# Kernel tuning notes

Hardware: AMD Instinct MI355X
Metric: run time of the kernel (lower is better)

## Reference

```python
import jax, jax.numpy as jnp
import numpy as np

BS = 2048   # batch, iterated sequentially (memory carried step to step)
M = 256     # memory_size
E = 128     # expanded_memory_emb_size
HS = 512    # summarizer_hidden_size
HA = 512    # shared_AC_hidden_size
HP = 256    # processor_hidden_size


def make_pe(max_len, d):
    # standard sinusoidal positional encoding [max_len, d]
    pos = np.arange(max_len, dtype=np.float32)[:, None]
    div = np.exp(np.arange(0, d, 2, dtype=np.float32) * (-np.log(10000.0) / d))
    pe = np.zeros((max_len, d), dtype=np.float32)
    pe[:, 0::2] = np.sin(pos * div)
    pe[:, 1::2] = np.cos(pos * div)
    return jnp.asarray(pe)


def setup_inputs() -> dict:
    key = jax.random.key(0)
    ks = jax.random.split(key, 32)

    def n(k, sh, s=0.05):
        return jax.random.normal(k, sh, dtype=jnp.float32) * s

    return {
        "state": jax.random.normal(ks[0], (BS, 4), dtype=jnp.float32),
        "memory0": jax.random.uniform(ks[1], (M, E), dtype=jnp.float32),  # buffer init U(0,1)
        # embedder: Linear(4, E)
        "W_emb": n(ks[2], (4, E)), "b_emb": n(ks[3], (E,)),
        # reader Summarizer MLP: E -> HS -> 1
        "Wr1": n(ks[4], (E, HS)), "br1": n(ks[5], (HS,)),
        "Wr2": n(ks[6], (HS, 1)), "br2": n(ks[7], (1,)),
        # writer Summarizer MLP: E -> HS -> M
        "Ww1": n(ks[8], (E, HS)), "bw1": n(ks[9], (HS,)),
        "Ww2": n(ks[10], (HS, M)), "bw2": n(ks[11], (M,)),
        # shared AC trunk: 2E -> HA
        "Ws": n(ks[12], (2 * E, HA)), "bs_": n(ks[13], (HA,)),
        # actor: HA -> 5, critic: HA -> 1
        "Wa": n(ks[14], (HA, 5)), "ba": n(ks[15], (5,)),
        "Wc": n(ks[16], (HA, 1)), "bc": n(ks[17], (1,)),
        # processor: (5 + 1 + 2E) -> HP -> E
        "Wp1": n(ks[18], (5 + 1 + 2 * E, HP)), "bp1": n(ks[19], (HP,)),
        "Wp2": n(ks[20], (HP, E)), "bp2": n(ks[21], (E,)),
    }


def reference(state, memory0, W_emb, b_emb, Wr1, br1, Wr2, br2,
              Ww1, bw1, Ww2, bw2, Ws, bs_, Wa, ba, Wc, bc,
              Wp1, bp1, Wp2, bp2):
    pe_mem = make_pe(M, E)  # PE added to the M memory slots
    sg = jax.lax.stop_gradient

    def summarize(x, W1, b1, W2, b2):
        # Summarizer (MLP method): weight = softmax over token axis, z = weight^T x
        w = jax.nn.softmax(jax.nn.relu(x @ W1 + b1) @ W2 + b2, axis=0)  # [T, K]
        return w.T @ x  # [K, E]

    se = state @ W_emb + b_emb  # embed once: [BS, E]

    def step(mem, s):
        # reader over [current state ; PE(memory)] -> single summary token
        xr = jnp.concatenate([s[None, :], mem + pe_mem], axis=0)        # [M+1, E]
        mem_state = summarize(xr, Wr1, br1, Wr2, br2)[0]                # [E]
        cstate = jnp.concatenate([s, mem_state])                        # concat=True -> [2E]
        h = jax.nn.relu(cstate @ Ws + bs_)                              # [HA]
        probs = jax.nn.softmax(h @ Wa + ba)                             # [5]
        val = h @ Wc + bc                                               # [1]
        pin = jnp.concatenate([s, mem_state, probs, val])               # [2E+6]
        ms2 = jax.nn.relu(pin @ Wp1 + bp1) @ Wp2 + bp2                  # processed mem_state [E]
        # writer sees detached state / mem_state / memory (torch .detach())
        xw = jnp.concatenate([sg(s)[None, :], sg(ms2)[None, :], sg(mem) + pe_mem], axis=0)  # [M+2, E]
        nm = summarize(xw, Ww1, bw1, Ww2, bw2)                          # [M, E]
        nm = nm - nm.min(axis=-1, keepdims=True)
        nm = nm / nm.max(axis=-1, keepdims=True)
        return nm, (probs, val)

    _, (action_probs, state_values) = jax.lax.scan(step, memory0, se)
    return action_probs, state_values  # [BS, 5], [BS, 1]
```

## Files before the change

### kernel.cpp

```cpp
#include <hip/hip_runtime.h>
#include <math.h>

#define BSZ 2048
#define MM  256
#define EE  128
#define HSS 512
#define HPP 256
#define NOWN 64
#define NBLK 129
#define LEADER 128
#define TPB 512
#define ROWS 4

typedef float f4 __attribute__((ext_vector_type(4)));

#define OFF_PE   512
#define OFF_R0   (OFF_PE + MM*EE)
#define OFF_W0   (OFF_R0 + BSZ)
#define OFF_MP   (OFF_W0 + BSZ*MM)
#define OFF_SW   (OFF_MP + 2*MM*EE)
#define OFF_EV   (OFF_SW + 2*MM*MM)
#define OFF_ES   (OFF_EV + NOWN*EE)
#define OFF_MS2  (OFF_ES + NOWN)
#define OFF_CS   (OFF_MS2 + EE)
#define OFF_CBS  (OFF_CS + 4*HSS)
#define OFF_CP   (OFF_CBS + HSS)
#define OFF_CBP  (OFF_CP + 4*HPP)
#define OFF_BD   (OFF_CBP + HPP)
#define OFF_BP   (OFF_BD + NOWN*ROWS)
#define OFF_PWR  (OFF_BP + NOWN*ROWS*EE)
#define OFF_PWW  (OFF_PWR + MM*HSS)
#define OFF_CSR  (OFF_PWW + MM*HSS)
#define OFF_CSW  (OFF_CSR + HSS)
#define OFF_CR   (OFF_CSW + HSS)
#define OFF_CBR  (OFF_CR + 4*HSS)
#define OFF_CW2  (OFF_CBR + HSS)
#define OFF_CBW  (OFF_CW2 + 4*HSS)
#define OFF_MSR  (OFF_CBW + HSS)
#define OFF_MSW  (OFF_MSR + 2*HSS)
#define OFF_SCAL (OFF_MSW + 2*HSS)

struct KParams {
  const float *state, *mem0, *Wemb, *bemb, *Wr1, *br1, *Wr2, *br2;
  const float *Ww1, *bw1, *Ww2, *bw2, *Ws, *bs, *Wa, *ba, *Wc, *bc;
  const float *Wp1, *bp1, *Wp2, *bp2;
  float *out;
  float *ws;
};

__device__ __forceinline__ float ldA(const float* p) {
  return __hip_atomic_load(p, __ATOMIC_RELAXED, __HIP_MEMORY_SCOPE_AGENT);
}
__device__ __forceinline__ void stA(float* p, float v) {
  __hip_atomic_store(p, v, __ATOMIC_RELAXED, __HIP_MEMORY_SCOPE_AGENT);
}
__device__ __forceinline__ unsigned ldAu(const unsigned* p) {
  return __hip_atomic_load(p, __ATOMIC_RELAXED, __HIP_MEMORY_SCOPE_AGENT);
}
__device__ __forceinline__ void stAu(unsigned* p, unsigned v) {
  __hip_atomic_store(p, v, __ATOMIC_RELAXED, __HIP_MEMORY_SCOPE_AGENT);
}

__device__ __forceinline__ void ldA4x8(const float* p, int strideF, f4* v) {
  const float *p1=p+strideF, *p2=p+2*strideF, *p3=p+3*strideF,
              *p4=p+4*strideF, *p5=p+5*strideF, *p6=p+6*strideF, *p7=p+7*strideF;
  asm volatile(
    "global_load_dwordx4 %0, %8, off sc0 sc1\n\t"
    "global_load_dwordx4 %1, %9, off sc0 sc1\n\t"
    "global_load_dwordx4 %2, %10, off sc0 sc1\n\t"
    "global_load_dwordx4 %3, %11, off sc0 sc1\n\t"
    "global_load_dwordx4 %4, %12, off sc0 sc1\n\t"
    "global_load_dwordx4 %5, %13, off sc0 sc1\n\t"
    "global_load_dwordx4 %6, %14, off sc0 sc1\n\t"
    "global_load_dwordx4 %7, %15, off sc0 sc1\n\t"
    "s_waitcnt vmcnt(0)"
    : "=&v"(v[0]), "=&v"(v[1]), "=&v"(v[2]), "=&v"(v[3]),
      "=&v"(v[4]), "=&v"(v[5]), "=&v"(v[6]), "=&v"(v[7])
    : "v"(p), "v"(p1), "v"(p2), "v"(p3), "v"(p4), "v"(p5), "v"(p6), "v"(p7)
    : "memory");
}
__device__ __forceinline__ void ldA4x4(const float* p, int strideF, f4* v) {
  const float *p1=p+strideF, *p2=p+2*strideF, *p3=p+3*strideF;
  asm volatile(
    "global_load_dwordx4 %0, %4, off sc0 sc1\n\t"
    "global_load_dwordx4 %1, %5, off sc0 sc1\n\t"
    "global_load_dwordx4 %2, %6, off sc0 sc1\n\t"
    "global_load_dwordx4 %3, %7, off sc0 sc1\n\t"
    "s_waitcnt vmcnt(0)"
    : "=&v"(v[0]), "=&v"(v[1]), "=&v"(v[2]), "=&v"(v[3])
    : "v"(p), "v"(p1), "v"(p2), "v"(p3)
    : "memory");
}
__device__ __forceinline__ f4 ldA4(const float* p) {
  f4 r;
  asm volatile("global_load_dwordx4 %0, %1, off sc0 sc1\n\ts_waitcnt vmcnt(0)"
    : "=&v"(r) : "v"(p) : "memory");
  return r;
}

__device__ __forceinline__ void drainSync() {
  asm volatile("s_waitcnt vmcnt(0)" ::: "memory");
  __syncthreads();
}

__device__ __forceinline__ float brs(float v, float* s8, int tid) {
  for (int o = 32; o > 0; o >>= 1) v += __shfl_down(v, o, 64);
  __syncthreads();
  if ((tid & 63) == 0) s8[tid >> 6] = v;
  __syncthreads();
  float r = s8[0]+s8[1]+s8[2]+s8[3]+s8[4]+s8[5]+s8[6]+s8[7];
  __syncthreads();
  return r;
}

template<int N>
__device__ __forceinline__ void brsN(float* v, float* sred, int tid) {
  #pragma unroll
  for (int k = 0; k < N; ++k)
    for (int o = 32; o > 0; o >>= 1) v[k] += __shfl_down(v[k], o, 64);
  __syncthreads();
  if ((tid & 63) == 0) {
    const int w = tid >> 6;
    #pragma unroll
    for (int k = 0; k < N; ++k) sred[k*8 + w] = v[k];
  }
  __syncthreads();
  #pragma unroll
  for (int k = 0; k < N; ++k) {
    float s = sred[k*8 + 0];
    #pragma unroll
    for (int w = 1; w < 8; ++w) s += sred[k*8 + w];
    v[k] = s;
  }
  __syncthreads();
}

__global__ __launch_bounds__(TPB)
void toyac_kernel(KParams p) {
  const int g = blockIdx.x;
  const int tid = threadIdx.x;
  float* ws = p.ws;
  unsigned* bar = (unsigned*)p.ws;
  const int og = (g >= NOWN && g < LEADER) ? (g - NOWN) : g;
  const int c0 = ROWS * ((g < NOWN) ? g : og);

  __shared__ float sBuf[8192];
  __shared__ float sX[ROWS][EE];
  __shared__ float sP[ROWS][EE];
  __shared__ float sPE[ROWS][EE];
  __shared__ float sPW[ROWS][HSS];
  __shared__ float sH4[ROWS][HSS];
  __shared__ float sMSR[HSS];
  __shared__ float sMSWv[HSS];
  __shared__ float sRed[16];
  __shared__ float s8[8];
  __shared__ float sR48[48];
  __shared__ float sMS[EE];
  __shared__ float sMS2[EE];
  __shared__ float sSE[EE];
  __shared__ float sP1[HPP];
  __shared__ float sD[ROWS];
  __shared__ float sSm[40];

  float (*sEv)[MM] = (float(*)[MM])sH4;
  float* sHv = &sH4[2][0];

  const int hq = (tid & 127) * 4;
  const int eg4 = tid >> 7;

  auto streamPW = [&](const float* W, float (*src)[EE]) {
    {
      f4 a0={0.f,0.f,0.f,0.f},a1=a0,a2=a0,a3=a0;
      const float* base = W + (size_t)(eg4*32)*HSS + hq;
      for (int i = 0; i < 32; ++i) {
        f4 w = *(const f4*)(base + (size_t)i*HSS);
        int e = eg4*32 + i;
        a0 += src[0][e]*w; a1 += src[1][e]*w; a2 += src[2][e]*w; a3 += src[3][e]*w;
      }
      *(f4*)(sBuf + ((size_t)eg4*ROWS + 0)*HSS + hq) = a0;
      *(f4*)(sBuf + ((size_t)eg4*ROWS + 1)*HSS + hq) = a1;
      *(f4*)(sBuf + ((size_t)eg4*ROWS + 2)*HSS + hq) = a2;
      *(f4*)(sBuf + ((size_t)eg4*ROWS + 3)*HSS + hq) = a3;
    }
    __syncthreads();
    #pragma unroll
    for (int r = 0; r < ROWS; ++r)
      sPW[r][tid] = sBuf[(0*ROWS+r)*HSS+tid] + sBuf[(1*ROWS+r)*HSS+tid]
                  + sBuf[(2*ROWS+r)*HSS+tid] + sBuf[(3*ROWS+r)*HSS+tid];
    __syncthreads();
  };

  if (g < NOWN) {
    const int e = tid & 127, r = tid >> 7, c = c0 + r;
    double dv = exp(-(double)(2*(e>>1)) * log(10000.0) / 128.0);
    double arg = (double)c * dv;
    float pev = ((e & 1) == 0) ? (float)sin(arg) : (float)cos(arg);
    stA(ws + OFF_PE + (size_t)c*EE + e, pev);
    sPE[r][e] = pev;
    float m0v = p.mem0[(size_t)c*EE + e] + pev;
    stA(ws + OFF_MP + (size_t)c*EE + e, m0v);
    sX[r][e] = m0v;
  } else if (g == LEADER) {
    for (int jj = tid; jj < HSS; jj += TPB) {
      float a0=0.f,a1=0.f,a2=0.f,a3=0.f,cb=0.f;
      for (int e = 0; e < EE; ++e) {
        float wv = p.Ws[(size_t)e*HSS + jj];
        a0 += p.Wemb[e]*wv; a1 += p.Wemb[EE+e]*wv;
        a2 += p.Wemb[2*EE+e]*wv; a3 += p.Wemb[3*EE+e]*wv;
        cb += p.bemb[e]*wv;
      }
      ws[OFF_CS + jj] = a0; ws[OFF_CS + HSS + jj] = a1;
      ws[OFF_CS + 2*HSS + jj] = a2; ws[OFF_CS + 3*HSS + jj] = a3;
      ws[OFF_CBS + jj] = cb;
    }
    if (tid < HPP) {
      int k = tid;
      float a0=0.f,a1=0.f,a2=0.f,a3=0.f,cb=0.f;
      for (int e = 0; e < EE; ++e) {
        float wv = p.Wp1[(size_t)e*HPP + k];
        a0 += p.Wemb[e]*wv; a1 += p.Wemb[EE+e]*wv;
        a2 += p.Wemb[2*EE+e]*wv; a3 += p.Wemb[3*EE+e]*wv;
        cb += p.bemb[e]*wv;
      }
      ws[OFF_CP + k] = a0; ws[OFF_CP + HPP + k] = a1;
      ws[OFF_CP + 2*HPP + k] = a2; ws[OFF_CP + 3*HPP + k] = a3;
      ws[OFF_CBP + k] = cb;
    }
    {
      int j = tid;
      float r0=0.f,r1=0.f,r2=0.f,r3=0.f,rb=0.f,rc=0.f;
      float w0=0.f,w1=0.f,w2=0.f,w3=0.f,wb=0.f,wc=0.f;
      for (int e = 0; e < EE; ++e) {
        float wr = p.Wr1[(size_t)e*HSS + j];
        float ww = p.Ww1[(size_t)e*HSS + j];
        float we0=p.Wemb[e], we1=p.Wemb[EE+e], we2=p.Wemb[2*EE+e], we3=p.Wemb[3*EE+e], wbe=p.bemb[e];
        r0+=we0*wr; r1+=we1*wr; r2+=we2*wr; r3+=we3*wr; rb+=wbe*wr; rc+=wr;
        w0+=we0*ww; w1+=we1*ww; w2+=we2*ww; w3+=we3*ww; wb+=wbe*ww; wc+=ww;
      }
      stA(ws+OFF_CR+j, r0); stA(ws+OFF_CR+HSS+j, r1);
      stA(ws+OFF_CR+2*HSS+j, r2); stA(ws+OFF_CR+3*HSS+j, r3);
      stA(ws+OFF_CBR+j, rb); stA(ws+OFF_CSR+j, rc);
      stA(ws+OFF_CW2+j, w0); stA(ws+OFF_CW2+HSS+j, w1);
      stA(ws+OFF_CW2+2*HSS+j, w2); stA(ws+OFF_CW2+3*HSS+j, w3);
      stA(ws+OFF_CBW+j, wb); stA(ws+OFF_CSW+j, wc);
    }
  }

  for (int t = g; t < BSZ; t += NBLK) {
    __syncthreads();
    if (tid < EE) {
      const float* st = p.state + (size_t)t*4;
      sSE[tid] = st[0]*p.Wemb[tid] + st[1]*p.Wemb[EE+tid]
               + st[2]*p.Wemb[2*EE+tid] + st[3]*p.Wemb[3*EE+tid] + p.bemb[tid];
    }
    __syncthreads();
    {
      f4 a = {0.f,0.f,0.f,0.f};
      const float* base = p.Wr1 + (size_t)(eg4*32)*HSS + hq;
      for (int i = 0; i < 32; ++i)
        a += sSE[eg4*32 + i] * (*(const f4*)(base + (size_t)i*HSS));
      *(f4*)(sBuf + (size_t)eg4*HSS + hq) = a;
      __syncthreads();
      int h = tid;
      float hid = sBuf[h] + sBuf[HSS+h] + sBuf[2*HSS+h] + sBuf[3*HSS+h] + p.br1[h];
      float v = fmaxf(hid, 0.f) * p.Wr2[h];
      float sc = brs(v, s8, tid);
      if (tid == 0) stA(ws + OFF_R0 + t, sc + p.br2[0]);
      __syncthreads();
    }
    {
      f4 a = {0.f,0.f,0.f,0.f};
      const float* base = p.Ww1 + (size_t)(eg4*32)*HSS + hq;
      for (int i = 0; i < 32; ++i)
        a += sSE[eg4*32 + i] * (*(const f4*)(base + (size_t)i*HSS));
      *(f4*)(sBuf + (size_t)eg4*HSS + hq) = a;
      __syncthreads();
      int h = tid;
      sHv[h] = fmaxf(sBuf[h] + sBuf[HSS+h] + sBuf[2*HSS+h] + sBuf[3*HSS+h] + p.bw1[h], 0.f);
      __syncthreads();
      const int cq = (tid & 63) * 4, hg = tid >> 6;
      f4 q = {0.f,0.f,0.f,0.f};
      const float* b2 = p.Ww2 + (size_t)(hg*64)*MM + cq;
      for (int i = 0; i < 64; ++i)
        q += sHv[hg*64 + i] * (*(const f4*)(b2 + (size_t)i*MM));
      *(f4*)(sBuf + (size_t)hg*MM + cq) = q;
      __syncthreads();
      if (tid < MM) {
        float s = 0.f;
        #pragma unroll
        for (int k = 0; k < 8; ++k) s += sBuf[(size_t)k*MM + tid];
        stA(ws + OFF_W0 + (size_t)t*MM + tid, s + p.bw2[tid]);
      }
      __syncthreads();
    }
  }

  auto stageA_full = [&]() {
    {
      f4 a0={0.f,0.f,0.f,0.f},a1=a0,a2=a0,a3=a0;
      const float* base = p.Wr1 + (size_t)(eg4*32)*HSS + hq;
      for (int i = 0; i < 32; ++i) {
        f4 w = *(const f4*)(base + (size_t)i*HSS);
        int e = eg4*32 + i;
        a0 += sX[0][e]*w; a1 += sX[1][e]*w; a2 += sX[2][e]*w; a3 += sX[3][e]*w;
      }
      *(f4*)(sBuf + ((size_t)eg4*ROWS + 0)*HSS + hq) = a0;
      *(f4*)(sBuf + ((size_t)eg4*ROWS + 1)*HSS + hq) = a1;
      *(f4*)(sBuf + ((size_t)eg4*ROWS + 2)*HSS + hq) = a2;
      *(f4*)(sBuf + ((size_t)eg4*ROWS + 3)*HSS + hq) = a3;
    }
    __syncthreads();
    float es[ROWS];
    {
      int h = tid;
      float b = p.br1[h], wr = p.Wr2[h];
      float sc[ROWS];
      #pragma unroll
      for (int r = 0; r < ROWS; ++r) {
        float hid = sBuf[(0*ROWS+r)*HSS+h] + sBuf[(1*ROWS+r)*HSS+h]
                  + sBuf[(2*ROWS+r)*HSS+h] + sBuf[(3*ROWS+r)*HSS+h] + b;
        sc[r] = fmaxf(hid, 0.f) * wr;
      }
      brsN<ROWS>(sc, sR48, tid);
      #pragma unroll
      for (int r = 0; r < ROWS; ++r) es[r] = expf(sc[r] + p.br2[0]);
    }
    if (tid < EE) {
      float v = es[0]*sX[0][tid] + es[1]*sX[1][tid] + es[2]*sX[2][tid] + es[3]*sX[3][tid];
      stA(ws + OFF_EV + (size_t)g*EE + tid, v);
    }
    if (tid == 0) stA(ws + OFF_ES + g, es[0]+es[1]+es[2]+es[3]);
  };

  auto ww2pass = [&](float* swdst) {
    const int cq = (tid & 63) * 4, hg = tid >> 6;
    f4 q0={0.f,0.f,0.f,0.f},q1=q0,q2=q0,q3=q0;
    const float* b2 = p.Ww2 + (size_t)(hg*64)*MM + cq;
    for (int i = 0; i < 64; ++i) {
      f4 w = *(const f4*)(b2 + (size_t)i*MM);
      int h = hg*64 + i;
      q0 += sH4[0][h]*w; q1 += sH4[1][h]*w; q2 += sH4[2][h]*w; q3 += sH4[3][h]*w;
    }
    *(f4*)(sBuf + ((size_t)hg*ROWS + 0)*MM + cq) = q0;
    *(f4*)(sBuf + ((size_t)hg*ROWS + 1)*MM + cq) = q1;
    *(f4*)(sBuf + ((size_t)hg*ROWS + 2)*MM + cq) = q2;
    *(f4*)(sBuf + ((size_t)hg*ROWS + 3)*MM + cq) = q3;
    __syncthreads();
    {
      const int col = tid & 255, rp = tid >> 8;
      #pragma unroll
      for (int rr = 0; rr < 2; ++rr) {
        int r = rp*2 + rr;
        float s = 0.f;
        #pragma unroll
        for (int k = 0; k < 8; ++k) s += sBuf[((size_t)k*ROWS + r)*MM + col];
        stA(swdst + (size_t)(c0 + r)*MM + col, s + p.bw2[col]);
      }
    }
  };

  auto stageC_full = [&](float* swdst) {
    {
      f4 a0={0.f,0.f,0.f,0.f},a1=a0,a2=a0,a3=a0;
      const float* base = p.Ww1 + (size_t)(eg4*32)*HSS + hq;
      for (int i = 0; i < 32; ++i) {
        f4 w = *(const f4*)(base + (size_t)i*HSS);
        int e = eg4*32 + i;
        a0 += sX[0][e]*w; a1 += sX[1][e]*w; a2 += sX[2][e]*w; a3 += sX[3][e]*w;
      }
      *(f4*)(sBuf + ((size_t)eg4*ROWS + 0)*HSS + hq) = a0;
      *(f4*)(sBuf + ((size_t)eg4*ROWS + 1)*HSS + hq) = a1;
      *(f4*)(sBuf + ((size_t)eg4*ROWS + 2)*HSS + hq) = a2;
      *(f4*)(sBuf + ((size_t)eg4*ROWS + 3)*HSS + hq) = a3;
    }
    __syncthreads();
    {
      int h = tid;
      float b = p.bw1[h];
      #pragma unroll
      for (int r = 0; r < ROWS; ++r)
        sH4[r][h] = fmaxf(sBuf[(0*ROWS+r)*HSS+h] + sBuf[(1*ROWS+r)*HSS+h]
                        + sBuf[(2*ROWS+r)*HSS+h] + sBuf[(3*ROWS+r)*HSS+h] + b, 0.f);
    }
    __syncthreads();
    ww2pass(swdst);
  };

  auto dBulkH = [&](int tt) {
    float* swc = ws + OFF_SW + (size_t)(tt&1)*MM*MM;
    float* mpc = ws + OFF_MP + (size_t)(tt&1)*MM*EE;
    float ex[ROWS] = {0.f,0.f,0.f,0.f};
    if (tid < MM) {
      f4 s = ldA4(swc + (size_t)tid*MM + c0);
      #pragma unroll
      for (int r = 0; r < ROWS; ++r) { ex[r] = expf(s[r]); sEv[r][tid] = ex[r]; }
    }
    brsN<ROWS>(ex, sR48, tid);
    if (tid == 0) {
      stA(ws + OFF_BD + og*ROWS + 0, ex[0]);
      stA(ws + OFF_BD + og*ROWS + 1, ex[1]);
      stA(ws + OFF_BD + og*ROWS + 2, ex[2]);
      stA(ws + OFF_BD + og*ROWS + 3, ex[3]);
    }
    {
      const int e4 = (tid & 31) * 4, rg = tid >> 5;
      f4 a0={0.f,0.f,0.f,0.f},a1=a0,a2=a0,a3=a0;
      const float* base = mpc + (size_t)(rg*16)*EE + e4;
      f4 vv[8];
      ldA4x8(base, EE, vv);
      #pragma unroll
      for (int i = 0; i < 8; ++i) {
        int r0 = rg*16 + i;
        a0 += sEv[0][r0]*vv[i]; a1 += sEv[1][r0]*vv[i];
        a2 += sEv[2][r0]*vv[i]; a3 += sEv[3][r0]*vv[i];
      }
      ldA4x8(base + 8*EE, EE, vv);
      #pragma unroll
      for (int i = 0; i < 8; ++i) {
        int r0 = rg*16 + 8 + i;
        a0 += sEv[0][r0]*vv[i]; a1 += sEv[1][r0]*vv[i];
        a2 += sEv[2][r0]*vv[i]; a3 += sEv[3][r0]*vv[i];
      }
      *(f4*)(sBuf + ((size_t)0*16 + rg)*EE + e4) = a0;
      *(f4*)(sBuf + ((size_t)1*16 + rg)*EE + e4) = a1;
      *(f4*)(sBuf + ((size_t)2*16 + rg)*EE + e4) = a2;
      *(f4*)(sBuf + ((size_t)3*16 + rg)*EE + e4) = a3;
    }
    __syncthreads();
    {
      const int e = tid & 127, r = tid >> 7;
      float s = 0.f;
      #pragma unroll
      for (int q = 0; q < 16; ++q) s += sBuf[((size_t)r*16 + q)*EE + e];
      sP[r][e] = s;
      stA(ws + OFF_BP + ((size_t)og*ROWS + r)*EE + e, s);
    }
    __syncthreads();
  };

  if (g == LEADER) {
    for (int t = 0; t < BSZ; ++t) {
      if (tid < NOWN) {
        while (ldAu(&bar[64+tid]) < (unsigned)(t+1)) __builtin_amdgcn_s_sleep(1);
      }
      __syncthreads();
      const float* st = p.state + (size_t)t*4;
      const float s0 = st[0], s1 = st[1], s2 = st[2], s3 = st[3];
      if (tid < EE)
        sSE[tid] = s0*p.Wemb[tid] + s1*p.Wemb[EE+tid]
                 + s2*p.Wemb[2*EE+tid] + s3*p.Wemb[3*EE+tid] + p.bemb[tid];
      float er0 = expf(ldA(ws + OFF_R0 + t));
      float v = (tid < NOWN) ? ldA(ws + OFF_ES + tid) : 0.f;
      float invd = 1.f / (er0 + brs(v, s8, tid));
      {
        const int e4 = (tid & 31) * 4, qg = tid >> 5;
        f4 vv[4];
        ldA4x4(ws + OFF_EV + (size_t)(qg*4)*EE + e4, EE, vv);
        f4 acc = vv[0]+vv[1]+vv[2]+vv[3];
        *(f4*)(sBuf + (size_t)qg*EE + e4) = acc;
      }
      __syncthreads();
      if (tid < EE) {
        float s = 0.f;
        #pragma unroll
        for (int q = 0; q < 16; ++q) s += sBuf[(size_t)q*EE + tid];
        sMS[tid] = (er0*sSE[tid] + s) * invd;
      }
      __syncthreads();
      {
        f4 a = {0.f,0.f,0.f,0.f};
        const float* base = p.Ws + (size_t)(EE + eg4*32)*HSS + hq;
        for (int i = 0; i < 32; ++i)
          a += sMS[eg4*32 + i] * (*(const f4*)(base + (size_t)i*HSS));
        *(f4*)(sBuf + (size_t)eg4*HSS + hq) = a;
      }
      __syncthreads();
      float hv;
      {
        int j = tid;
        const float* cs = ws + OFF_CS;
        float sh0 = s0*cs[j] + s1*cs[HSS+j] + s2*cs[2*HSS+j] + s3*cs[3*HSS+j] + ws[OFF_CBS + j];
        hv = fmaxf(sBuf[j] + sBuf[HSS+j] + sBuf[2*HSS+j] + sBuf[3*HSS+j] + sh0 + p.bs[j], 0.f);
      }
      __syncthreads();
      {
        int j = tid;
        float pa[6];
        #pragma unroll
        for (int aa = 0; aa < 5; ++aa) pa[aa] = hv * p.Wa[(size_t)j*5 + aa];
        pa[5] = hv * p.Wc[j];
        brsN<6>(pa, sR48, tid);
        if (tid == 0) {
          float l0=pa[0]+p.ba[0], l1=pa[1]+p.ba[1], l2=pa[2]+p.ba[2];
          float l3=pa[3]+p.ba[3], l4=pa[4]+p.ba[4];
          float mx = fmaxf(fmaxf(fmaxf(l0,l1),fmaxf(l2,l3)), l4);
          float e0=expf(l0-mx),e1=expf(l1-mx),e2=expf(l2-mx),e3=expf(l3-mx),e4v=expf(l4-mx);
          float is = 1.f/(e0+e1+e2+e3+e4v);
          float p0=e0*is,p1=e1*is,p2=e2*is,p3=e3*is,p4=e4v*is;
          p.out[(size_t)t*5+0]=p0; p.out[(size_t)t*5+1]=p1; p.out[(size_t)t*5+2]=p2;
          p.out[(size_t)t*5+3]=p3; p.out[(size_t)t*5+4]=p4;
          float val = pa[5] + p.bc[0];
          p.out[(size_t)BSZ*5 + t] = val;
          sSm[1]=p0; sSm[2]=p1; sSm[3]=p2; sSm[4]=p3; sSm[5]=p4; sSm[6]=val;
        }
        __syncthreads();
      }
      {
        const int cq = (tid & 63) * 4, eg8 = tid >> 6;
        f4 a = {0.f,0.f,0.f,0.f};
        const float* base = p.Wp1 + (size_t)(EE + eg8*16)*HPP + cq;
        for (int i = 0; i < 16; ++i)
          a += sMS[eg8*16 + i] * (*(const f4*)(base + (size_t)i*HPP));
        *(f4*)(sBuf + (size_t)eg8*HPP + cq) = a;
      }
      __syncthreads();
      if (tid < HPP) {
        int k = tid;
        const float* cp = ws + OFF_CP;
        float acc = s0*cp[k] + s1*cp[HPP+k] + s2*cp[2*HPP+k] + s3*cp[3*HPP+k]
                  + ws[OFF_CBP + k] + p.bp1[k];
        #pragma unroll
        for (int q = 0; q < 8; ++q) acc += sBuf[(size_t)q*HPP + k];
        #pragma unroll
        for (int aa = 0; aa < 5; ++aa) acc += sSm[1+aa] * p.Wp1[(size_t)(2*EE+aa)*HPP + k];
        acc += sSm[6] * p.Wp1[(size_t)(2*EE+5)*HPP + k];
        sP1[k] = fmaxf(acc, 0.f);
      }
      __syncthreads();
      {
        const int cq = (tid & 31) * 4, kg = tid >> 5;
        f4 a = {0.f,0.f,0.f,0.f};
        const float* base = p.Wp2 + (size_t)(kg*16)*EE + cq;
        for (int i = 0; i < 16; ++i)
          a += sP1[kg*16 + i] * (*(const f4*)(base + (size_t)i*EE));
        *(f4*)(sBuf + (size_t)kg*EE + cq) = a;
      }
      __syncthreads();
      if (tid < EE) {
        float s = 0.f;
        #pragma unroll
        for (int q = 0; q < 16; ++q) s += sBuf[(size_t)q*EE + tid];
        stA(ws + OFF_MS2 + tid, s + p.bp2[tid]);
      }
      drainSync();
      if (tid == 0) stAu(&bar[320], (unsigned)(t+1));
    }
  } else if (g < NOWN) {
    const f4 wcol = *(const f4*)(p.Ww2 + (size_t)tid*MM + c0);
    drainSync();
    if (tid == 0) stAu(&bar[g], 1u);
    streamPW(p.Wr1, sPE);
    #pragma unroll
    for (int r = 0; r < ROWS; ++r)
      ws[OFF_PWR + (size_t)(c0+r)*HSS + tid] = sPW[r][tid];
    __syncthreads();
    stageA_full();
    drainSync();
    if (tid == 0) stAu(&bar[64+g], 1u);

    for (int t = 0; t < BSZ-1; ++t) {
      if (tid == 0) {
        while (ldAu(&bar[320]) < (unsigned)(t+1)) __builtin_amdgcn_s_sleep(1);
      }
      __syncthreads();
      if (tid < EE) sMS2[tid] = ldA(ws + OFF_MS2 + tid);
      __syncthreads();
      {
        const int h8 = tid >> 6, ee = tid & 63;
        const int h = 8*g + h8;
        float m1 = sMS2[ee], m2 = sMS2[ee+64];
        float pr = m1*p.Wr1[(size_t)ee*HSS+h] + m2*p.Wr1[(size_t)(ee+64)*HSS+h];
        float pw = m1*p.Ww1[(size_t)ee*HSS+h] + m2*p.Ww1[(size_t)(ee+64)*HSS+h];
        for (int o = 32; o > 0; o >>= 1) {
          pr += __shfl_down(pr, o, 64);
          pw += __shfl_down(pw, o, 64);
        }
        if (ee == 0) {
          stA(ws + OFF_MSR + (size_t)(t&1)*HSS + h, pr);
          stA(ws + OFF_MSW + (size_t)(t&1)*HSS + h, pw);
        }
      }
      drainSync();
      if (tid == 0) stAu(&bar[256+g], (unsigned)(t+1));
      if (tid == 0) {
        while (ldAu(&bar[192+g]) < (unsigned)(t+1)) __builtin_amdgcn_s_sleep(1);
      }
      __syncthreads();
      if (tid == 0) {
        f4 d = ldA4(ws + OFF_BD + g*ROWS);
        sD[0]=d.x; sD[1]=d.y; sD[2]=d.z; sD[3]=d.w;
        f4 w0 = ldA4(ws + OFF_W0 + (size_t)t*MM + c0);
        sSm[8+0]=expf(w0.x); sSm[8+1]=expf(w0.y); sSm[8+2]=expf(w0.z); sSm[8+3]=expf(w0.w);
      }
      {
        const int e = tid & 127, r = tid >> 7;
        sP[r][e] = ldA(ws + OFF_BP + ((size_t)g*ROWS + r)*EE + e);
      }
      __syncthreads();
      streamPW(p.Wr1, sP);
      if (tid < NOWN) {
        while (ldAu(&bar[256+tid]) < (unsigned)(t+1)) __builtin_amdgcn_s_sleep(1);
      }
      __syncthreads();
      sMSR[tid]  = ldA(ws + OFF_MSR + (size_t)(t&1)*HSS + tid);
      sMSWv[tid] = ldA(ws + OFF_MSW + (size_t)(t&1)*HSS + tid);
      __syncthreads();
      float swv[ROWS];
      {
        float hm = fmaxf(sMSWv[tid] + p.bw1[tid], 0.f);
        swv[0]=hm*wcol.x; swv[1]=hm*wcol.y; swv[2]=hm*wcol.z; swv[3]=hm*wcol.w;
        brsN<ROWS>(swv, sR48, tid);
      }
      const float* st = p.state + (size_t)t*4;
      {
        const int e = tid & 127, r = tid >> 7;
        float ew1 = expf(swv[r] + p.bw2[c0+r]);
        float ew0 = sSm[8+r];
        float inv = 1.f / (sD[r] + ew0 + ew1);
        float se = st[0]*p.Wemb[e] + st[1]*p.Wemb[EE+e]
                 + st[2]*p.Wemb[2*EE+e] + st[3]*p.Wemb[3*EE+e] + p.bemb[e];
        float x = (sP[r][e] + ew0*se + ew1*sMS2[e]) * inv;
        float mn = x, mx = x;
        #pragma unroll
        for (int o = 1; o < 64; o <<= 1) {
          mn = fminf(mn, __shfl_xor(mn, o, 64));
          mx = fmaxf(mx, __shfl_xor(mx, o, 64));
        }
        if ((tid & 63) == 0) { sRed[(tid>>6)*2] = mn; sRed[(tid>>6)*2+1] = mx; }
        __syncthreads();
        mn = fminf(sRed[4*r], sRed[4*r+2]);
        mx = fmaxf(sRed[4*r+1], sRed[4*r+3]);
        float k = 1.f / (mx - mn);
        float xr = (x - mn) * k + sPE[r][e];
        float* mpn = ws + OFF_MP + (size_t)((t+1)&1)*MM*EE;
        stA(mpn + (size_t)(c0+r)*EE + e, xr);
        sX[r][e] = xr;
        if (tid < 4) {
          int rr = tid;
          float ew1b = expf(swv[rr] + p.bw2[c0+rr]);
          float invb = 1.f / (sD[rr] + sSm[8+rr] + ew1b);
          float mnb = fminf(sRed[4*rr], sRed[4*rr+2]);
          float mxb = fmaxf(sRed[4*rr+1], sRed[4*rr+3]);
          float kb = 1.f / (mxb - mnb);
          float a = kb * invb;
          float b = a * sSm[8+rr];
          float c = a * ew1b;
          float d = -mnb * kb;
          stA(ws + OFF_SCAL + (size_t)(c0+rr)*4 + 0, a);
          stA(ws + OFF_SCAL + (size_t)(c0+rr)*4 + 1, b);
          stA(ws + OFF_SCAL + (size_t)(c0+rr)*4 + 2, c);
          stA(ws + OFF_SCAL + (size_t)(c0+rr)*4 + 3, d);
          sSm[16+rr*4+0]=a; sSm[16+rr*4+1]=b; sSm[16+rr*4+2]=c; sSm[16+rr*4+3]=d;
        }
      }
      drainSync();
      if (tid == 0) stAu(&bar[g], (unsigned)(t+2));
      {
        const int j = tid;
        float seW = st[0]*ldA(ws+OFF_CR+j) + st[1]*ldA(ws+OFF_CR+HSS+j)
                  + st[2]*ldA(ws+OFF_CR+2*HSS+j) + st[3]*ldA(ws+OFF_CR+3*HSS+j)
                  + ldA(ws+OFF_CBR+j);
        float csv = ldA(ws+OFF_CSR+j);
        float br = p.br1[j], wr = p.Wr2[j];
        float sc[ROWS];
        #pragma unroll
        for (int r = 0; r < ROWS; ++r) {
          float pre = sSm[16+r*4+0]*sPW[r][j] + sSm[16+r*4+1]*seW
                    + sSm[16+r*4+2]*sMSR[j] + sSm[16+r*4+3]*csv
                    + ws[OFF_PWR + (size_t)(c0+r)*HSS + j] + br;
          sc[r] = fmaxf(pre, 0.f) * wr;
        }
        brsN<ROWS>(sc, sR48, tid);
        float es[ROWS];
        #pragma unroll
        for (int r = 0; r < ROWS; ++r) es[r] = expf(sc[r] + p.br2[0]);
        if (tid < EE) {
          float v = es[0]*sX[0][tid] + es[1]*sX[1][tid] + es[2]*sX[2][tid] + es[3]*sX[3][tid];
          stA(ws + OFF_EV + (size_t)g*EE + tid, v);
        }
        if (tid == 0) stA(ws + OFF_ES + g, es[0]+es[1]+es[2]+es[3]);
      }
      drainSync();
      if (tid == 0) stAu(&bar[64+g], (unsigned)(t+2));
    }
  } else {
    if (tid == 0) {
      while (ldAu(&bar[og]) < 1u) __builtin_amdgcn_s_sleep(1);
    }
    __syncthreads();
    {
      const int e = tid & 127, r = tid >> 7;
      sPE[r][e] = ldA(ws + OFF_PE + (size_t)(c0+r)*EE + e);
      sX[r][e]  = ldA(ws + OFF_MP + (size_t)(c0+r)*EE + e);
    }
    __syncthreads();
    streamPW(p.Ww1, sPE);
    #pragma unroll
    for (int r = 0; r < ROWS; ++r)
      ws[OFF_PWW + (size_t)(c0+r)*HSS + tid] = sPW[r][tid];
    __syncthreads();
    stageC_full(ws + OFF_SW);
    drainSync();
    if (tid == 0) stAu(&bar[128+og], 1u);
    if (tid < 64) {
      while (ldAu(&bar[128+tid]) < 1u) __builtin_amdgcn_s_sleep(1);
    } else if (tid < 128) {
      while (ldAu(&bar[tid-64]) < 1u) __builtin_amdgcn_s_sleep(1);
    }
    __syncthreads();
    dBulkH(0);
    drainSync();
    if (tid == 0) stAu(&bar[192+og], 1u);
    streamPW(p.Ww1, sP);

    for (int t = 0; t < BSZ-2; ++t) {
      if (tid < NOWN) {
        while (ldAu(&bar[256+tid]) < (unsigned)(t+1)) __builtin_amdgcn_s_sleep(1);
      }
      __syncthreads();
      sMSWv[tid] = ldA(ws + OFF_MSW + (size_t)(t&1)*HSS + tid);
      if (tid == 0) {
        while (ldAu(&bar[og]) < (unsigned)(t+2)) __builtin_amdgcn_s_sleep(1);
      }
      __syncthreads();
      if (tid < 16) sSm[16+tid] = ldA(ws + OFF_SCAL + (size_t)c0*4 + tid);
      __syncthreads();
      {
        const int j = tid;
        const float* st = p.state + (size_t)t*4;
        float seW = st[0]*ldA(ws+OFF_CW2+j) + st[1]*ldA(ws+OFF_CW2+HSS+j)
                  + st[2]*ldA(ws+OFF_CW2+2*HSS+j) + st[3]*ldA(ws+OFF_CW2+3*HSS+j)
                  + ldA(ws+OFF_CBW+j);
        float csv = ldA(ws+OFF_CSW+j);
        float bw = p.bw1[j];
        #pragma unroll
        for (int r = 0; r < ROWS; ++r) {
          float pre = sSm[16+r*4+0]*sPW[r][j] + sSm[16+r*4+1]*seW
                    + sSm[16+r*4+2]*sMSWv[j] + sSm[16+r*4+3]*csv
                    + ws[OFF_PWW + (size_t)(c0+r)*HSS + j] + bw;
          sH4[r][j] = fmaxf(pre, 0.f);
        }
      }
      __syncthreads();
      ww2pass(ws + OFF_SW + (size_t)((t+1)&1)*MM*MM);
      drainSync();
      if (tid == 0) stAu(&bar[128+og], (unsigned)(t+2));
      if (tid < 64) {
        while (ldAu(&bar[128+tid]) < (unsigned)(t+2)) __builtin_amdgcn_s_sleep(1);
      } else if (tid < 128) {
        while (ldAu(&bar[tid-64]) < (unsigned)(t+2)) __builtin_amdgcn_s_sleep(1);
      }
      __syncthreads();
      dBulkH(t+1);
      drainSync();
      if (tid == 0) stAu(&bar[192+og], (unsigned)(t+2));
      streamPW(p.Ww1, sP);
    }
  }
}

extern "C" void kernel_launch(void* const* d_in, const int* in_sizes, int n_in,
                              void* d_out, int out_size, void* d_ws, size_t ws_size,
                              hipStream_t stream) {
  hipMemsetAsync(d_ws, 0, 2048, stream);
  KParams kp;
  kp.state = (const float*)d_in[0];
  kp.mem0  = (const float*)d_in[1];
  kp.Wemb  = (const float*)d_in[2];
  kp.bemb  = (const float*)d_in[3];
  kp.Wr1   = (const float*)d_in[4];
  kp.br1   = (const float*)d_in[5];
  kp.Wr2   = (const float*)d_in[6];
  kp.br2   = (const float*)d_in[7];
  kp.Ww1   = (const float*)d_in[8];
  kp.bw1   = (const float*)d_in[9];
  kp.Ww2   = (const float*)d_in[10];
  kp.bw2   = (const float*)d_in[11];
  kp.Ws    = (const float*)d_in[12];
  kp.bs    = (const float*)d_in[13];
  kp.Wa    = (const float*)d_in[14];
  kp.ba    = (const float*)d_in[15];
  kp.Wc    = (const float*)d_in[16];
  kp.bc    = (const float*)d_in[17];
  kp.Wp1   = (const float*)d_in[18];
  kp.bp1   = (const float*)d_in[19];
  kp.Wp2   = (const float*)d_in[20];
  kp.bp2   = (const float*)d_in[21];
  kp.out   = (float*)d_out;
  kp.ws    = (float*)d_ws;
  toyac_kernel<<<dim3(NBLK), dim3(TPB), 0, stream>>>(kp);
}
```

Measured before the change: 57.19 ms.

## Remove leader block, replicate controller in owners, offload reader projection to helpers

Drops the dedicated leader block so every owner block recomputes the per-step actor-critic/processor path redundantly, with block 0 writing outputs. The reader's projection of P through Wr1 moves to the helper blocks, which publish it in a new workspace buffer. EV/ES become double-buffered and the per-step constants are hoisted into registers. The intent is to remove the leader-to-owner barrier hop from each sequential step's critical path. In exchange, every owner does redundant work and the barrier protocol is reorganised, which risks new ordering bugs.

```diff
diff --git a/kernel.cpp b/kernel.cpp
--- a/kernel.cpp
+++ b/kernel.cpp
@@ -7,38 +7,37 @@
 #define HSS 512
 #define HPP 256
 #define NOWN 64
-#define NBLK 129
-#define LEADER 128
+#define NBLK 128
 #define TPB 512
 #define ROWS 4
 
 typedef float f4 __attribute__((ext_vector_type(4)));
 
-#define OFF_PE   512
-#define OFF_R0   (OFF_PE + MM*EE)
-#define OFF_W0   (OFF_R0 + BSZ)
-#define OFF_MP   (OFF_W0 + BSZ*MM)
-#define OFF_SW   (OFF_MP + 2*MM*EE)
-#define OFF_EV   (OFF_SW + 2*MM*MM)
-#define OFF_ES   (OFF_EV + NOWN*EE)
-#define OFF_MS2  (OFF_ES + NOWN)
-#define OFF_CS   (OFF_MS2 + EE)
-#define OFF_CBS  (OFF_CS + 4*HSS)
-#define OFF_CP   (OFF_CBS + HSS)
-#define OFF_CBP  (OFF_CP + 4*HPP)
-#define OFF_BD   (OFF_CBP + HPP)
-#define OFF_BP   (OFF_BD + NOWN*ROWS)
-#define OFF_PWR  (OFF_BP + NOWN*ROWS*EE)
-#define OFF_PWW  (OFF_PWR + MM*HSS)
-#define OFF_CSR  (OFF_PWW + MM*HSS)
-#define OFF_CSW  (OFF_CSR + HSS)
-#define OFF_CR   (OFF_CSW + HSS)
-#define OFF_CBR  (OFF_CR + 4*HSS)
-#define OFF_CW2  (OFF_CBR + HSS)
-#define OFF_CBW  (OFF_CW2 + 4*HSS)
-#define OFF_MSR  (OFF_CBW + HSS)
-#define OFF_MSW  (OFF_MSR + 2*HSS)
-#define OFF_SCAL (OFF_MSW + 2*HSS)
+#define OFF_PE    512
+#define OFF_R0    (OFF_PE + MM*EE)
+#define OFF_W0    (OFF_R0 + BSZ)
+#define OFF_MP    (OFF_W0 + BSZ*MM)
+#define OFF_SW    (OFF_MP + 2*MM*EE)
+#define OFF_EV    (OFF_SW + 2*MM*MM)
+#define OFF_ES    (OFF_EV + 2*NOWN*EE)
+#define OFF_CS    (OFF_ES + 2*NOWN)
+#define OFF_CBS   (OFF_CS + 4*HSS)
+#define OFF_CP    (OFF_CBS + HSS)
+#define OFF_CBP   (OFF_CP + 4*HPP)
+#define OFF_CR    (OFF_CBP + HPP)
+#define OFF_CBR   (OFF_CR + 4*HSS)
+#define OFF_CSR   (OFF_CBR + HSS)
+#define OFF_CW2   (OFF_CSR + HSS)
+#define OFF_CBW   (OFF_CW2 + 4*HSS)
+#define OFF_CSW   (OFF_CBW + HSS)
+#define OFF_BD    (OFF_CSW + HSS)
+#define OFF_BP    (OFF_BD + NOWN*ROWS)
+#define OFF_PWRD  (OFF_BP + NOWN*ROWS*EE)
+#define OFF_PWRpe (OFF_PWRD + NOWN*ROWS*HSS)
+#define OFF_PWWpe (OFF_PWRpe + MM*HSS)
+#define OFF_MSR   (OFF_PWWpe + MM*HSS)
+#define OFF_MSW   (OFF_MSR + 2*HSS)
+#define OFF_SCAL  (OFF_MSW + 2*HSS)
 
 struct KParams {
   const float *state, *mem0, *Wemb, *bemb, *Wr1, *br1, *Wr2, *br2;
@@ -141,29 +140,30 @@
   const int tid = threadIdx.x;
   float* ws = p.ws;
   unsigned* bar = (unsigned*)p.ws;
-  const int og = (g >= NOWN && g < LEADER) ? (g - NOWN) : g;
-  const int c0 = ROWS * ((g < NOWN) ? g : og);
+  const int isOwner = (g < NOWN);
+  const int og = isOwner ? g : (g - NOWN);
+  const int c0 = ROWS * og;
 
   __shared__ float sBuf[8192];
+  __shared__ float sPW[ROWS][HSS];
+  __shared__ float sH4[ROWS][HSS];
   __shared__ float sX[ROWS][EE];
   __shared__ float sP[ROWS][EE];
   __shared__ float sPE[ROWS][EE];
-  __shared__ float sPW[ROWS][HSS];
-  __shared__ float sH4[ROWS][HSS];
   __shared__ float sMSR[HSS];
   __shared__ float sMSWv[HSS];
-  __shared__ float sRed[16];
-  __shared__ float s8[8];
-  __shared__ float sR48[48];
   __shared__ float sMS[EE];
   __shared__ float sMS2[EE];
   __shared__ float sSE[EE];
   __shared__ float sP1[HPP];
   __shared__ float sD[ROWS];
+  __shared__ float sR48[48];
+  __shared__ float s8[8];
+  __shared__ float sRed[16];
   __shared__ float sSm[40];
 
   float (*sEv)[MM] = (float(*)[MM])sH4;
-  float* sHv = &sH4[2][0];
+  float* sHv = sMSR;
 
   const int hq = (tid & 127) * 4;
   const int eg4 = tid >> 7;
@@ -190,7 +190,7 @@
     __syncthreads();
   };
 
-  if (g < NOWN) {
+  if (isOwner) {
     const int e = tid & 127, r = tid >> 7, c = c0 + r;
     double dv = exp(-(double)(2*(e>>1)) * log(10000.0) / 128.0);
     double arg = (double)c * dv;
@@ -200,49 +200,50 @@
     float m0v = p.mem0[(size_t)c*EE + e] + pev;
     stA(ws + OFF_MP + (size_t)c*EE + e, m0v);
     sX[r][e] = m0v;
-  } else if (g == LEADER) {
-    for (int jj = tid; jj < HSS; jj += TPB) {
-      float a0=0.f,a1=0.f,a2=0.f,a3=0.f,cb=0.f;
-      for (int e = 0; e < EE; ++e) {
-        float wv = p.Ws[(size_t)e*HSS + jj];
-        a0 += p.Wemb[e]*wv; a1 += p.Wemb[EE+e]*wv;
-        a2 += p.Wemb[2*EE+e]*wv; a3 += p.Wemb[3*EE+e]*wv;
-        cb += p.bemb[e]*wv;
-      }
-      ws[OFF_CS + jj] = a0; ws[OFF_CS + HSS + jj] = a1;
-      ws[OFF_CS + 2*HSS + jj] = a2; ws[OFF_CS + 3*HSS + jj] = a3;
-      ws[OFF_CBS + jj] = cb;
-    }
-    if (tid < HPP) {
-      int k = tid;
-      float a0=0.f,a1=0.f,a2=0.f,a3=0.f,cb=0.f;
-      for (int e = 0; e < EE; ++e) {
-        float wv = p.Wp1[(size_t)e*HPP + k];
-        a0 += p.Wemb[e]*wv; a1 += p.Wemb[EE+e]*wv;
-        a2 += p.Wemb[2*EE+e]*wv; a3 += p.Wemb[3*EE+e]*wv;
-        cb += p.bemb[e]*wv;
-      }
-      ws[OFF_CP + k] = a0; ws[OFF_CP + HPP + k] = a1;
-      ws[OFF_CP + 2*HPP + k] = a2; ws[OFF_CP + 3*HPP + k] = a3;
-      ws[OFF_CBP + k] = cb;
-    }
-    {
+    if (g == 0) {
       int j = tid;
-      float r0=0.f,r1=0.f,r2=0.f,r3=0.f,rb=0.f,rc=0.f;
-      float w0=0.f,w1=0.f,w2=0.f,w3=0.f,wb=0.f,wc=0.f;
-      for (int e = 0; e < EE; ++e) {
-        float wr = p.Wr1[(size_t)e*HSS + j];
-        float ww = p.Ww1[(size_t)e*HSS + j];
-        float we0=p.Wemb[e], we1=p.Wemb[EE+e], we2=p.Wemb[2*EE+e], we3=p.Wemb[3*EE+e], wbe=p.bemb[e];
-        r0+=we0*wr; r1+=we1*wr; r2+=we2*wr; r3+=we3*wr; rb+=wbe*wr; rc+=wr;
-        w0+=we0*ww; w1+=we1*ww; w2+=we2*ww; w3+=we3*ww; wb+=wbe*ww; wc+=ww;
-      }
-      stA(ws+OFF_CR+j, r0); stA(ws+OFF_CR+HSS+j, r1);
-      stA(ws+OFF_CR+2*HSS+j, r2); stA(ws+OFF_CR+3*HSS+j, r3);
-      stA(ws+OFF_CBR+j, rb); stA(ws+OFF_CSR+j, rc);
-      stA(ws+OFF_CW2+j, w0); stA(ws+OFF_CW2+HSS+j, w1);
-      stA(ws+OFF_CW2+2*HSS+j, w2); stA(ws+OFF_CW2+3*HSS+j, w3);
-      stA(ws+OFF_CBW+j, wb); stA(ws+OFF_CSW+j, wc);
+      {
+        float a0=0.f,a1=0.f,a2=0.f,a3=0.f,cb=0.f;
+        for (int ee = 0; ee < EE; ++ee) {
+          float wv = p.Ws[(size_t)ee*HSS + j];
+          a0 += p.Wemb[ee]*wv; a1 += p.Wemb[EE+ee]*wv;
+          a2 += p.Wemb[2*EE+ee]*wv; a3 += p.Wemb[3*EE+ee]*wv;
+          cb += p.bemb[ee]*wv;
+        }
+        stA(ws+OFF_CS+j, a0); stA(ws+OFF_CS+HSS+j, a1);
+        stA(ws+OFF_CS+2*HSS+j, a2); stA(ws+OFF_CS+3*HSS+j, a3);
+        stA(ws+OFF_CBS+j, cb);
+      }
+      {
+        float r0=0.f,r1=0.f,r2=0.f,r3=0.f,rb=0.f,rc=0.f;
+        float w0=0.f,w1=0.f,w2=0.f,w3=0.f,wb=0.f,wc=0.f;
+        for (int ee = 0; ee < EE; ++ee) {
+          float wr = p.Wr1[(size_t)ee*HSS + j];
+          float wwv = p.Ww1[(size_t)ee*HSS + j];
+          float we0=p.Wemb[ee], we1=p.Wemb[EE+ee], we2=p.Wemb[2*EE+ee], we3=p.Wemb[3*EE+ee], wbe=p.bemb[ee];
+          r0+=we0*wr; r1+=we1*wr; r2+=we2*wr; r3+=we3*wr; rb+=wbe*wr; rc+=wr;
+          w0+=we0*wwv; w1+=we1*wwv; w2+=we2*wwv; w3+=we3*wwv; wb+=wbe*wwv; wc+=wwv;
+        }
+        stA(ws+OFF_CR+j, r0); stA(ws+OFF_CR+HSS+j, r1);
+        stA(ws+OFF_CR+2*HSS+j, r2); stA(ws+OFF_CR+3*HSS+j, r3);
+        stA(ws+OFF_CBR+j, rb); stA(ws+OFF_CSR+j, rc);
+        stA(ws+OFF_CW2+j, w0); stA(ws+OFF_CW2+HSS+j, w1);
+        stA(ws+OFF_CW2+2*HSS+j, w2); stA(ws+OFF_CW2+3*HSS+j, w3);
+        stA(ws+OFF_CBW+j, wb); stA(ws+OFF_CSW+j, wc);
+      }
+      if (tid < HPP) {
+        int k = tid;
+        float a0=0.f,a1=0.f,a2=0.f,a3=0.f,cb=0.f;
+        for (int ee = 0; ee < EE; ++ee) {
+          float wv = p.Wp1[(size_t)ee*HPP + k];
+          a0 += p.Wemb[ee]*wv; a1 += p.Wemb[EE+ee]*wv;
+          a2 += p.Wemb[2*EE+ee]*wv; a3 += p.Wemb[3*EE+ee]*wv;
+          cb += p.bemb[ee]*wv;
+        }
+        stA(ws+OFF_CP+k, a0); stA(ws+OFF_CP+HPP+k, a1);
+        stA(ws+OFF_CP+2*HPP+k, a2); stA(ws+OFF_CP+3*HPP+k, a3);
+        stA(ws+OFF_CBP+k, cb);
+      }
     }
   }
 
@@ -294,43 +295,6 @@
       __syncthreads();
     }
   }
-
-  auto stageA_full = [&]() {
-    {
-      f4 a0={0.f,0.f,0.f,0.f},a1=a0,a2=a0,a3=a0;
-      const float* base = p.Wr1 + (size_t)(eg4*32)*HSS + hq;
-      for (int i = 0; i < 32; ++i) {
-        f4 w = *(const f4*)(base + (size_t)i*HSS);
-        int e = eg4*32 + i;
-        a0 += sX[0][e]*w; a1 += sX[1][e]*w; a2 += sX[2][e]*w; a3 += sX[3][e]*w;
-      }
-      *(f4*)(sBuf + ((size_t)eg4*ROWS + 0)*HSS + hq) = a0;
-      *(f4*)(sBuf + ((size_t)eg4*ROWS + 1)*HSS + hq) = a1;
-      *(f4*)(sBuf + ((size_t)eg4*ROWS + 2)*HSS + hq) = a2;
-      *(f4*)(sBuf + ((size_t)eg4*ROWS + 3)*HSS + hq) = a3;
-    }
-    __syncthreads();
-    float es[ROWS];
-    {
-      int h = tid;
-      float b = p.br1[h], wr = p.Wr2[h];
-      float sc[ROWS];
-      #pragma unroll
-      for (int r = 0; r < ROWS; ++r) {
-        float hid = sBuf[(0*ROWS+r)*HSS+h] + sBuf[(1*ROWS+r)*HSS+h]
-                  + sBuf[(2*ROWS+r)*HSS+h] + sBuf[(3*ROWS+r)*HSS+h] + b;
-        sc[r] = fmaxf(hid, 0.f) * wr;
-      }
-      brsN<ROWS>(sc, sR48, tid);
-      #pragma unroll
-      for (int r = 0; r < ROWS; ++r) es[r] = expf(sc[r] + p.br2[0]);
-    }
-    if (tid < EE) {
-      float v = es[0]*sX[0][tid] + es[1]*sX[1][tid] + es[2]*sX[2][tid] + es[3]*sX[3][tid];
-      stA(ws + OFF_EV + (size_t)g*EE + tid, v);
-    }
-    if (tid == 0) stA(ws + OFF_ES + g, es[0]+es[1]+es[2]+es[3]);
-  };
 
   auto ww2pass = [&](float* swdst) {
     const int cq = (tid & 63) * 4, hg = tid >> 6;
@@ -359,33 +323,6 @@
     }
   };
 
-  auto stageC_full = [&](float* swdst) {
-    {
-      f4 a0={0.f,0.f,0.f,0.f},a1=a0,a2=a0,a3=a0;
-      const float* base = p.Ww1 + (size_t)(eg4*32)*HSS + hq;
-      for (int i = 0; i < 32; ++i) {
-        f4 w = *(const f4*)(base + (size_t)i*HSS);
-        int e = eg4*32 + i;
-        a0 += sX[0][e]*w; a1 += sX[1][e]*w; a2 += sX[2][e]*w; a3 += sX[3][e]*w;
-      }
-      *(f4*)(sBuf + ((size_t)eg4*ROWS + 0)*HSS + hq) = a0;
-      *(f4*)(sBuf + ((size_t)eg4*ROWS + 1)*HSS + hq) = a1;
-      *(f4*)(sBuf + ((size_t)eg4*ROWS + 2)*HSS + hq) = a2;
-      *(f4*)(sBuf + ((size_t)eg4*ROWS + 3)*HSS + hq) = a3;
-    }
-    __syncthreads();
-    {
-      int h = tid;
-      float b = p.bw1[h];
-      #pragma unroll
-      for (int r = 0; r < ROWS; ++r)
-        sH4[r][h] = fmaxf(sBuf[(0*ROWS+r)*HSS+h] + sBuf[(1*ROWS+r)*HSS+h]
-                        + sBuf[(2*ROWS+r)*HSS+h] + sBuf[(3*ROWS+r)*HSS+h] + b, 0.f);
-    }
-    __syncthreads();
-    ww2pass(swdst);
-  };
-
   auto dBulkH = [&](int tt) {
     float* swc = ws + OFF_SW + (size_t)(tt&1)*MM*MM;
     float* mpc = ws + OFF_MP + (size_t)(tt&1)*MM*EE;
@@ -438,11 +375,70 @@
     __syncthreads();
   };
 
-  if (g == LEADER) {
+  if (isOwner) {
+    const f4 wcol = *(const f4*)(p.Ww2 + (size_t)tid*MM + c0);
+    const float rBr1 = p.br1[tid], rWr2 = p.Wr2[tid], rBw1v = p.bw1[tid];
+    drainSync();
+    if (tid == 0) stAu(&bar[128+g], 1u);
+    streamPW(p.Wr1, sPE);
+    float rPWRpe[ROWS];
+    #pragma unroll
+    for (int r = 0; r < ROWS; ++r) {
+      ws[OFF_PWRpe + (size_t)(c0+r)*HSS + tid] = sPW[r][tid];
+      rPWRpe[r] = sPW[r][tid];
+    }
+    __syncthreads();
+    {
+      {
+        f4 a0={0.f,0.f,0.f,0.f},a1=a0,a2=a0,a3=a0;
+        const float* base = p.Wr1 + (size_t)(eg4*32)*HSS + hq;
+        for (int i = 0; i < 32; ++i) {
+          f4 w = *(const f4*)(base + (size_t)i*HSS);
+          int e = eg4*32 + i;
+          a0 += sX[0][e]*w; a1 += sX[1][e]*w; a2 += sX[2][e]*w; a3 += sX[3][e]*w;
+        }
+        *(f4*)(sBuf + ((size_t)eg4*ROWS + 0)*HSS + hq) = a0;
+        *(f4*)(sBuf + ((size_t)eg4*ROWS + 1)*HSS + hq) = a1;
+        *(f4*)(sBuf + ((size_t)eg4*ROWS + 2)*HSS + hq) = a2;
+        *(f4*)(sBuf + ((size_t)eg4*ROWS + 3)*HSS + hq) = a3;
+      }
+      __syncthreads();
+      float sc[ROWS];
+      #pragma unroll
+      for (int r = 0; r < ROWS; ++r) {
+        float hid = sBuf[(0*ROWS+r)*HSS+tid] + sBuf[(1*ROWS+r)*HSS+tid]
+                  + sBuf[(2*ROWS+r)*HSS+tid] + sBuf[(3*ROWS+r)*HSS+tid] + rBr1;
+        sc[r] = fmaxf(hid, 0.f) * rWr2;
+      }
+      brsN<ROWS>(sc, sR48, tid);
+      float es[ROWS];
+      #pragma unroll
+      for (int r = 0; r < ROWS; ++r) es[r] = expf(sc[r] + p.br2[0]);
+      if (tid < EE) {
+        float v = es[0]*sX[0][tid] + es[1]*sX[1][tid] + es[2]*sX[2][tid] + es[3]*sX[3][tid];
+        stA(ws + OFF_EV + (size_t)g*EE + tid, v);
+      }
+      if (tid == 0) stA(ws + OFF_ES + g, es[0]+es[1]+es[2]+es[3]);
+    }
+    drainSync();
+    if (tid == 0) stAu(&bar[g], 1u);
+    if (tid < NOWN) { while (ldAu(&bar[tid]) < 1u) __builtin_amdgcn_s_sleep(1); }
+    __syncthreads();
+    const float rCS0=ldA(ws+OFF_CS+tid), rCS1=ldA(ws+OFF_CS+HSS+tid),
+                rCS2=ldA(ws+OFF_CS+2*HSS+tid), rCS3=ldA(ws+OFF_CS+3*HSS+tid),
+                rCBS=ldA(ws+OFF_CBS+tid);
+    const float rCR0=ldA(ws+OFF_CR+tid), rCR1=ldA(ws+OFF_CR+HSS+tid),
+                rCR2=ldA(ws+OFF_CR+2*HSS+tid), rCR3=ldA(ws+OFF_CR+3*HSS+tid),
+                rCBR=ldA(ws+OFF_CBR+tid), rCSR=ldA(ws+OFF_CSR+tid);
+    float rCP0=0,rCP1=0,rCP2=0,rCP3=0,rCBP=0;
+    if (tid < HPP) {
+      rCP0=ldA(ws+OFF_CP+tid); rCP1=ldA(ws+OFF_CP+HPP+tid);
+      rCP2=ldA(ws+OFF_CP+2*HPP+tid); rCP3=ldA(ws+OFF_CP+3*HPP+tid);
+      rCBP=ldA(ws+OFF_CBP+tid);
+    }
+
     for (int t = 0; t < BSZ; ++t) {
-      if (tid < NOWN) {
-        while (ldAu(&bar[64+tid]) < (unsigned)(t+1)) __builtin_amdgcn_s_sleep(1);
-      }
+      if (tid < NOWN) { while (ldAu(&bar[tid]) < (unsigned)(t+1)) __builtin_amdgcn_s_sleep(1); }
       __syncthreads();
       const float* st = p.state + (size_t)t*4;
       const float s0 = st[0], s1 = st[1], s2 = st[2], s3 = st[3];
@@ -450,12 +446,12 @@
         sSE[tid] = s0*p.Wemb[tid] + s1*p.Wemb[EE+tid]
                  + s2*p.Wemb[2*EE+tid] + s3*p.Wemb[3*EE+tid] + p.bemb[tid];
       float er0 = expf(ldA(ws + OFF_R0 + t));
-      float v = (tid < NOWN) ? ldA(ws + OFF_ES + tid) : 0.f;
+      float v = (tid < NOWN) ? ldA(ws + OFF_ES + (size_t)(t&1)*NOWN + tid) : 0.f;
       float invd = 1.f / (er0 + brs(v, s8, tid));
       {
         const int e4 = (tid & 31) * 4, qg = tid >> 5;
         f4 vv[4];
-        ldA4x4(ws + OFF_EV + (size_t)(qg*4)*EE + e4, EE, vv);
+        ldA4x4(ws + OFF_EV + (size_t)(t&1)*NOWN*EE + (size_t)(qg*4)*EE + e4, EE, vv);
         f4 acc = vv[0]+vv[1]+vv[2]+vv[3];
         *(f4*)(sBuf + (size_t)qg*EE + e4) = acc;
       }
@@ -477,18 +473,16 @@
       __syncthreads();
       float hv;
       {
-        int j = tid;
-        const float* cs = ws + OFF_CS;
-        float sh0 = s0*cs[j] + s1*cs[HSS+j] + s2*cs[2*HSS+j] + s3*cs[3*HSS+j] + ws[OFF_CBS + j];
-        hv = fmaxf(sBuf[j] + sBuf[HSS+j] + sBuf[2*HSS+j] + sBuf[3*HSS+j] + sh0 + p.bs[j], 0.f);
-      }
-      __syncthreads();
-      {
-        int j = tid;
+        float sh0 = s0*rCS0 + s1*rCS1 + s2*rCS2 + s3*rCS3 + rCBS;
+        hv = fmaxf(sBuf[tid] + sBuf[HSS+tid] + sBuf[2*HSS+tid] + sBuf[3*HSS+tid]
+                   + sh0 + p.bs[tid], 0.f);
+      }
+      __syncthreads();
+      {
         float pa[6];
         #pragma unroll
-        for (int aa = 0; aa < 5; ++aa) pa[aa] = hv * p.Wa[(size_t)j*5 + aa];
-        pa[5] = hv * p.Wc[j];
+        for (int aa = 0; aa < 5; ++aa) pa[aa] = hv * p.Wa[(size_t)tid*5 + aa];
+        pa[5] = hv * p.Wc[tid];
         brsN<6>(pa, sR48, tid);
         if (tid == 0) {
           float l0=pa[0]+p.ba[0], l1=pa[1]+p.ba[1], l2=pa[2]+p.ba[2];
@@ -497,11 +491,12 @@
           float e0=expf(l0-mx),e1=expf(l1-mx),e2=expf(l2-mx),e3=expf(l3-mx),e4v=expf(l4-mx);
           float is = 1.f/(e0+e1+e2+e3+e4v);
           float p0=e0*is,p1=e1*is,p2=e2*is,p3=e3*is,p4=e4v*is;
-          p.out[(size_t)t*5+0]=p0; p.out[(size_t)t*5+1]=p1; p.out[(size_t)t*5+2]=p2;
-          p.out[(size_t)t*5+3]=p3; p.out[(size_t)t*5+4]=p4;
-          float val = pa[5] + p.bc[0];
-          p.out[(size_t)BSZ*5 + t] = val;
-          sSm[1]=p0; sSm[2]=p1; sSm[3]=p2; sSm[4]=p3; sSm[5]=p4; sSm[6]=val;
+          if (g == 0) {
+            p.out[(size_t)t*5+0]=p0; p.out[(size_t)t*5+1]=p1; p.out[(size_t)t*5+2]=p2;
+            p.out[(size_t)t*5+3]=p3; p.out[(size_t)t*5+4]=p4;
+            p.out[(size_t)BSZ*5 + t] = pa[5] + p.bc[0];
+          }
+          sSm[1]=p0; sSm[2]=p1; sSm[3]=p2; sSm[4]=p3; sSm[5]=p4; sSm[6]=pa[5]+p.bc[0];
         }
         __syncthreads();
       }
@@ -515,16 +510,13 @@
       }
       __syncthreads();
       if (tid < HPP) {
-        int k = tid;
-        const float* cp = ws + OFF_CP;
-        float acc = s0*cp[k] + s1*cp[HPP+k] + s2*cp[2*HPP+k] + s3*cp[3*HPP+k]
-                  + ws[OFF_CBP + k] + p.bp1[k];
-        #pragma unroll
-        for (int q = 0; q < 8; ++q) acc += sBuf[(size_t)q*HPP + k];
-        #pragma unroll
-        for (int aa = 0; aa < 5; ++aa) acc += sSm[1+aa] * p.Wp1[(size_t)(2*EE+aa)*HPP + k];
-        acc += sSm[6] * p.Wp1[(size_t)(2*EE+5)*HPP + k];
-        sP1[k] = fmaxf(acc, 0.f);
+        float acc = s0*rCP0 + s1*rCP1 + s2*rCP2 + s3*rCP3 + rCBP + p.bp1[tid];
+        #pragma unroll
+        for (int q = 0; q < 8; ++q) acc += sBuf[(size_t)q*HPP + tid];
+        #pragma unroll
+        for (int aa = 0; aa < 5; ++aa) acc += sSm[1+aa] * p.Wp1[(size_t)(2*EE+aa)*HPP + tid];
+        acc += sSm[6] * p.Wp1[(size_t)(2*EE+5)*HPP + tid];
+        sP1[tid] = fmaxf(acc, 0.f);
       }
       __syncthreads();
       {
@@ -540,31 +532,10 @@
         float s = 0.f;
         #pragma unroll
         for (int q = 0; q < 16; ++q) s += sBuf[(size_t)q*EE + tid];
-        stA(ws + OFF_MS2 + tid, s + p.bp2[tid]);
-      }
-      drainSync();
-      if (tid == 0) stAu(&bar[320], (unsigned)(t+1));
-    }
-  } else if (g < NOWN) {
-    const f4 wcol = *(const f4*)(p.Ww2 + (size_t)tid*MM + c0);
-    drainSync();
-    if (tid == 0) stAu(&bar[g], 1u);
-    streamPW(p.Wr1, sPE);
-    #pragma unroll
-    for (int r = 0; r < ROWS; ++r)
-      ws[OFF_PWR + (size_t)(c0+r)*HSS + tid] = sPW[r][tid];
-    __syncthreads();
-    stageA_full();
-    drainSync();
-    if (tid == 0) stAu(&bar[64+g], 1u);
-
-    for (int t = 0; t < BSZ-1; ++t) {
-      if (tid == 0) {
-        while (ldAu(&bar[320]) < (unsigned)(t+1)) __builtin_amdgcn_s_sleep(1);
-      }
-      __syncthreads();
-      if (tid < EE) sMS2[tid] = ldA(ws + OFF_MS2 + tid);
-      __syncthreads();
+        sMS2[tid] = s + p.bp2[tid];
+      }
+      __syncthreads();
+      if (t == BSZ-1) break;
       {
         const int h8 = tid >> 6, ee = tid & 63;
         const int h = 8*g + h8;
@@ -581,45 +552,42 @@
         }
       }
       drainSync();
-      if (tid == 0) stAu(&bar[256+g], (unsigned)(t+1));
+      if (tid == 0) stAu(&bar[64+g], (unsigned)(t+1));
       if (tid == 0) {
-        while (ldAu(&bar[192+g]) < (unsigned)(t+1)) __builtin_amdgcn_s_sleep(1);
-      }
+        f4 w0 = ldA4(ws + OFF_W0 + (size_t)t*MM + c0);
+        sSm[8+0]=expf(w0.x); sSm[8+1]=expf(w0.y); sSm[8+2]=expf(w0.z); sSm[8+3]=expf(w0.w);
+      }
+      if (tid < NOWN) { while (ldAu(&bar[64+tid]) < (unsigned)(t+1)) __builtin_amdgcn_s_sleep(1); }
+      __syncthreads();
+      sMSR[tid]  = ldA(ws + OFF_MSR + (size_t)(t&1)*HSS + tid);
+      sMSWv[tid] = ldA(ws + OFF_MSW + (size_t)(t&1)*HSS + tid);
+      __syncthreads();
+      float swv[ROWS];
+      {
+        float hm = fmaxf(sMSWv[tid] + rBw1v, 0.f);
+        swv[0]=hm*wcol.x; swv[1]=hm*wcol.y; swv[2]=hm*wcol.z; swv[3]=hm*wcol.w;
+        brsN<ROWS>(swv, sR48, tid);
+      }
+      if (tid == 0) { while (ldAu(&bar[256+g]) < (unsigned)(t+1)) __builtin_amdgcn_s_sleep(1); }
       __syncthreads();
       if (tid == 0) {
         f4 d = ldA4(ws + OFF_BD + g*ROWS);
         sD[0]=d.x; sD[1]=d.y; sD[2]=d.z; sD[3]=d.w;
-        f4 w0 = ldA4(ws + OFF_W0 + (size_t)t*MM + c0);
-        sSm[8+0]=expf(w0.x); sSm[8+1]=expf(w0.y); sSm[8+2]=expf(w0.z); sSm[8+3]=expf(w0.w);
       }
       {
         const int e = tid & 127, r = tid >> 7;
         sP[r][e] = ldA(ws + OFF_BP + ((size_t)g*ROWS + r)*EE + e);
       }
-      __syncthreads();
-      streamPW(p.Wr1, sP);
-      if (tid < NOWN) {
-        while (ldAu(&bar[256+tid]) < (unsigned)(t+1)) __builtin_amdgcn_s_sleep(1);
-      }
-      __syncthreads();
-      sMSR[tid]  = ldA(ws + OFF_MSR + (size_t)(t&1)*HSS + tid);
-      sMSWv[tid] = ldA(ws + OFF_MSW + (size_t)(t&1)*HSS + tid);
-      __syncthreads();
-      float swv[ROWS];
-      {
-        float hm = fmaxf(sMSWv[tid] + p.bw1[tid], 0.f);
-        swv[0]=hm*wcol.x; swv[1]=hm*wcol.y; swv[2]=hm*wcol.z; swv[3]=hm*wcol.w;
-        brsN<ROWS>(swv, sR48, tid);
-      }
-      const float* st = p.state + (size_t)t*4;
+      #pragma unroll
+      for (int r = 0; r < ROWS; ++r)
+        sPW[r][tid] = ldA(ws + OFF_PWRD + ((size_t)g*ROWS + r)*HSS + tid);
+      __syncthreads();
       {
         const int e = tid & 127, r = tid >> 7;
         float ew1 = expf(swv[r] + p.bw2[c0+r]);
         float ew0 = sSm[8+r];
         float inv = 1.f / (sD[r] + ew0 + ew1);
-        float se = st[0]*p.Wemb[e] + st[1]*p.Wemb[EE+e]
-                 + st[2]*p.Wemb[2*EE+e] + st[3]*p.Wemb[3*EE+e] + p.bemb[e];
-        float x = (sP[r][e] + ew0*se + ew1*sMS2[e]) * inv;
+        float x = (sP[r][e] + ew0*sSE[e] + ew1*sMS2[e]) * inv;
         float mn = x, mx = x;
         #pragma unroll
         for (int o = 1; o < 64; o <<= 1) {
@@ -632,8 +600,7 @@
         mx = fmaxf(sRed[4*r+1], sRed[4*r+3]);
         float k = 1.f / (mx - mn);
         float xr = (x - mn) * k + sPE[r][e];
-        float* mpn = ws + OFF_MP + (size_t)((t+1)&1)*MM*EE;
-        stA(mpn + (size_t)(c0+r)*EE + e, xr);
+        stA(ws + OFF_MP + (size_t)((t+1)&1)*MM*EE + (size_t)(c0+r)*EE + e, xr);
         sX[r][e] = xr;
         if (tid < 4) {
           int rr = tid;
@@ -654,39 +621,33 @@
         }
       }
       drainSync();
-      if (tid == 0) stAu(&bar[g], (unsigned)(t+2));
-      {
-        const int j = tid;
-        float seW = st[0]*ldA(ws+OFF_CR+j) + st[1]*ldA(ws+OFF_CR+HSS+j)
-                  + st[2]*ldA(ws+OFF_CR+2*HSS+j) + st[3]*ldA(ws+OFF_CR+3*HSS+j)
-                  + ldA(ws+OFF_CBR+j);
-        float csv = ldA(ws+OFF_CSR+j);
-        float br = p.br1[j], wr = p.Wr2[j];
+      if (tid == 0) stAu(&bar[128+g], (unsigned)(t+2));
+      {
+        float seW = s0*rCR0 + s1*rCR1 + s2*rCR2 + s3*rCR3 + rCBR;
         float sc[ROWS];
         #pragma unroll
         for (int r = 0; r < ROWS; ++r) {
-          float pre = sSm[16+r*4+0]*sPW[r][j] + sSm[16+r*4+1]*seW
-                    + sSm[16+r*4+2]*sMSR[j] + sSm[16+r*4+3]*csv
-                    + ws[OFF_PWR + (size_t)(c0+r)*HSS + j] + br;
-          sc[r] = fmaxf(pre, 0.f) * wr;
+          float pre = sSm[16+r*4+0]*sPW[r][tid] + sSm[16+r*4+1]*seW
+                    + sSm[16+r*4+2]*sMSR[tid] + sSm[16+r*4+3]*rCSR
+                    + rPWRpe[r] + rBr1;
+          sc[r] = fmaxf(pre, 0.f) * rWr2;
         }
         brsN<ROWS>(sc, sR48, tid);
         float es[ROWS];
         #pragma unroll
         for (int r = 0; r < ROWS; ++r) es[r] = expf(sc[r] + p.br2[0]);
         if (tid < EE) {
-          float v = es[0]*sX[0][tid] + es[1]*sX[1][tid] + es[2]*sX[2][tid] + es[3]*sX[3][tid];
-          stA(ws + OFF_EV + (size_t)g*EE + tid, v);
-        }
-        if (tid == 0) stA(ws + OFF_ES + g, es[0]+es[1]+es[2]+es[3]);
+          float vv = es[0]*sX[0][tid] + es[1]*sX[1][tid] + es[2]*sX[2][tid] + es[3]*sX[3][tid];
+          stA(ws + OFF_EV + (size_t)((t+1)&1)*NOWN*EE + (size_t)g*EE + tid, vv);
+        }
+        if (tid == 0) stA(ws + OFF_ES + (size_t)((t+1)&1)*NOWN + g, es[0]+es[1]+es[2]+es[3]);
       }
       drainSync();
-      if (tid == 0) stAu(&bar[64+g], (unsigned)(t+2));
+      if (tid == 0) stAu(&bar[g], (unsigned)(t+2));
     }
   } else {
-    if (tid == 0) {
-      while (ldAu(&bar[og]) < 1u) __builtin_amdgcn_s_sleep(1);
-    }
+    const float rBw1 = p.bw1[tid];
+    if (tid == 0) { while (ldAu(&bar[128+og]) < 1u) __builtin_amdgcn_s_sleep(1); }
     __syncthreads();
     {
       const int e = tid & 127, r = tid >> 7;
@@ -695,65 +656,85 @@
     }
     __syncthreads();
     streamPW(p.Ww1, sPE);
+    float rPWWpe[ROWS];
+    #pragma unroll
+    for (int r = 0; r < ROWS; ++r) {
+      ws[OFF_PWWpe + (size_t)(c0+r)*HSS + tid] = sPW[r][tid];
+      rPWWpe[r] = sPW[r][tid];
+    }
+    __syncthreads();
+    {
+      {
+        f4 a0={0.f,0.f,0.f,0.f},a1=a0,a2=a0,a3=a0;
+        const float* base = p.Ww1 + (size_t)(eg4*32)*HSS + hq;
+        for (int i = 0; i < 32; ++i) {
+          f4 w = *(const f4*)(base + (size_t)i*HSS);
+          int e = eg4*32 + i;
+          a0 += sX[0][e]*w; a1 += sX[1][e]*w; a2 += sX[2][e]*w; a3 += sX[3][e]*w;
+        }
+        *(f4*)(sBuf + ((size_t)eg4*ROWS + 0)*HSS + hq) = a0;
+        *(f4*)(sBuf + ((size_t)eg4*ROWS + 1)*HSS + hq) = a1;
+        *(f4*)(sBuf + ((size_t)eg4*ROWS + 2)*HSS + hq) = a2;
+        *(f4*)(sBuf + ((size_t)eg4*ROWS + 3)*HSS + hq) = a3;
+      }
+      __syncthreads();
+      #pragma unroll
+      for (int r = 0; r < ROWS; ++r)
+        sH4[r][tid] = fmaxf(sBuf[(0*ROWS+r)*HSS+tid] + sBuf[(1*ROWS+r)*HSS+tid]
+                          + sBuf[(2*ROWS+r)*HSS+tid] + sBuf[(3*ROWS+r)*HSS+tid] + rBw1, 0.f);
+      __syncthreads();
+      ww2pass(ws + OFF_SW);
+    }
+    drainSync();
+    if (tid == 0) stAu(&bar[192+og], 1u);
+    if (tid < 64) { while (ldAu(&bar[192+tid]) < 1u) __builtin_amdgcn_s_sleep(1); }
+    else if (tid < 128) { while (ldAu(&bar[128+tid-64]) < 1u) __builtin_amdgcn_s_sleep(1); }
+    __syncthreads();
+    const float rCW0=ldA(ws+OFF_CW2+tid), rCW1=ldA(ws+OFF_CW2+HSS+tid),
+                rCW2v=ldA(ws+OFF_CW2+2*HSS+tid), rCW3=ldA(ws+OFF_CW2+3*HSS+tid),
+                rCBW=ldA(ws+OFF_CBW+tid), rCSW=ldA(ws+OFF_CSW+tid);
+    dBulkH(0);
+    streamPW(p.Wr1, sP);
     #pragma unroll
     for (int r = 0; r < ROWS; ++r)
-      ws[OFF_PWW + (size_t)(c0+r)*HSS + tid] = sPW[r][tid];
-    __syncthreads();
-    stageC_full(ws + OFF_SW);
+      stA(ws + OFF_PWRD + ((size_t)og*ROWS + r)*HSS + tid, sPW[r][tid]);
     drainSync();
-    if (tid == 0) stAu(&bar[128+og], 1u);
-    if (tid < 64) {
-      while (ldAu(&bar[128+tid]) < 1u) __builtin_amdgcn_s_sleep(1);
-    } else if (tid < 128) {
-      while (ldAu(&bar[tid-64]) < 1u) __builtin_amdgcn_s_sleep(1);
-    }
-    __syncthreads();
-    dBulkH(0);
-    drainSync();
-    if (tid == 0) stAu(&bar[192+og], 1u);
+    if (tid == 0) stAu(&bar[256+og], 1u);
     streamPW(p.Ww1, sP);
 
     for (int t = 0; t < BSZ-2; ++t) {
-      if (tid < NOWN) {
-        while (ldAu(&bar[256+tid]) < (unsigned)(t+1)) __builtin_amdgcn_s_sleep(1);
-      }
+      if (tid < 64) { while (ldAu(&bar[64+tid]) < (unsigned)(t+1)) __builtin_amdgcn_s_sleep(1); }
       __syncthreads();
       sMSWv[tid] = ldA(ws + OFF_MSW + (size_t)(t&1)*HSS + tid);
-      if (tid == 0) {
-        while (ldAu(&bar[og]) < (unsigned)(t+2)) __builtin_amdgcn_s_sleep(1);
-      }
+      if (tid == 0) { while (ldAu(&bar[128+og]) < (unsigned)(t+2)) __builtin_amdgcn_s_sleep(1); }
       __syncthreads();
       if (tid < 16) sSm[16+tid] = ldA(ws + OFF_SCAL + (size_t)c0*4 + tid);
       __syncthreads();
       {
-        const int j = tid;
         const float* st = p.state + (size_t)t*4;
-        float seW = st[0]*ldA(ws+OFF_CW2+j) + st[1]*ldA(ws+OFF_CW2+HSS+j)
-                  + st[2]*ldA(ws+OFF_CW2+2*HSS+j) + st[3]*ldA(ws+OFF_CW2+3*HSS+j)
-                  + ldA(ws+OFF_CBW+j);
-        float csv = ldA(ws+OFF_CSW+j);
-        float bw = p.bw1[j];
+        float seW = st[0]*rCW0 + st[1]*rCW1 + st[2]*rCW2v + st[3]*rCW3 + rCBW;
         #pragma unroll
         for (int r = 0; r < ROWS; ++r) {
-          float pre = sSm[16+r*4+0]*sPW[r][j] + sSm[16+r*4+1]*seW
-                    + sSm[16+r*4+2]*sMSWv[j] + sSm[16+r*4+3]*csv
-                    + ws[OFF_PWW + (size_t)(c0+r)*HSS + j] + bw;
-          sH4[r][j] = fmaxf(pre, 0.f);
+          float pre = sSm[16+r*4+0]*sPW[r][tid] + sSm[16+r*4+1]*seW
+                    + sSm[16+r*4+2]*sMSWv[tid] + sSm[16+r*4+3]*rCSW
+                    + rPWWpe[r] + rBw1;
+          sH4[r][tid] = fmaxf(pre, 0.f);
         }
       }
       __syncthreads();
       ww2pass(ws + OFF_SW + (size_t)((t+1)&1)*MM*MM);
       drainSync();
-      if (tid == 0) stAu(&bar[128+og], (unsigned)(t+2));
-      if (tid < 64) {
-        while (ldAu(&bar[128+tid]) < (unsigned)(t+2)) __builtin_amdgcn_s_sleep(1);
-      } else if (tid < 128) {
-        while (ldAu(&bar[tid-64]) < (unsigned)(t+2)) __builtin_amdgcn_s_sleep(1);
-      }
+      if (tid == 0) stAu(&bar[192+og], (unsigned)(t+2));
+      if (tid < 64) { while (ldAu(&bar[192+tid]) < (unsigned)(t+2)) __builtin_amdgcn_s_sleep(1); }
+      else if (tid < 128) { while (ldAu(&bar[128+tid-64]) < (unsigned)(t+2)) __builtin_amdgcn_s_sleep(1); }
       __syncthreads();
       dBulkH(t+1);
+      streamPW(p.Wr1, sP);
+      #pragma unroll
+      for (int r = 0; r < ROWS; ++r)
+        stA(ws + OFF_PWRD + ((size_t)og*ROWS + r)*HSS + tid, sPW[r][tid]);
       drainSync();
-      if (tid == 0) stAu(&bar[192+og], (unsigned)(t+2));
+      if (tid == 0) stAu(&bar[256+og], (unsigned)(t+2));
       streamPW(p.Ww1, sP);
     }
   }
```

Measured after the change: 61.58 ms. 7.7% more time.
